# Performance work log

Measured on AMD Instinct MI355X. Metric: run time of the kernel, lower is better.

## Reference

```python
import jax, jax.numpy as jnp
import numpy as np
import math

B, T, C, H, L, V = 8, 511, 1024, 16, 8, 128  # T = block_size - 1
D = C // H
FF = 4 * C


def setup_inputs() -> dict:
    key = jax.random.key(0)
    ks = jax.random.split(key, 12)
    std = 0.02
    n = lambda k, s: (jax.random.normal(k, s, dtype=jnp.float32) * std)
    idx = jax.random.randint(ks[0], (B, T), 0, V)
    idx = jnp.where(idx == 2, 3, idx)  # avoid pad token so logits[idx!=2] keeps all rows
    return {
        "idx": idx,
        "tok_emb": n(ks[1], (V, C)),
        "pos_emb": n(ks[2], (T, C)),
        "ln1_w": jnp.ones((L, C)), "ln1_b": jnp.zeros((L, C)),
        "Wq": n(ks[3], (L, C, C)), "bq": jnp.zeros((L, C)),
        "Wk": n(ks[4], (L, C, C)), "bk": jnp.zeros((L, C)),
        "Wv": n(ks[5], (L, C, C)), "bv": jnp.zeros((L, C)),
        "Wp": n(ks[6], (L, C, C)), "bp": jnp.zeros((L, C)),
        "ln2_w": jnp.ones((L, C)), "ln2_b": jnp.zeros((L, C)),
        "W1": n(ks[7], (L, C, FF)), "b1": jnp.zeros((L, FF)),
        "W2": n(ks[8], (L, FF, C)), "b2": jnp.zeros((L, C)),
        "lnf_w": jnp.ones((C,)), "lnf_b": jnp.zeros((C,)),
        "head_w": n(ks[9], (V, C)),
    }


def _ln(x, w, b):
    m = x.mean(-1, keepdims=True)
    v = ((x - m) ** 2).mean(-1, keepdims=True)
    return (x - m) * jax.lax.rsqrt(v + 1e-5) * w + b


def reference(idx, tok_emb, pos_emb, ln1_w, ln1_b, Wq, bq, Wk, bk, Wv, bv, Wp, bp,
              ln2_w, ln2_b, W1, b1, W2, b2, lnf_w, lnf_b, head_w):
    x = tok_emb[idx] + pos_emb[None, :, :]                      # [B,T,C]
    mask = jnp.tril(jnp.ones((T, T), dtype=bool))
    scale = 1.0 / math.sqrt(D)

    def block(x, p):
        h = _ln(x, p["ln1_w"], p["ln1_b"])
        q = (h @ p["Wq"] + p["bq"]).reshape(B, T, H, D).transpose(0, 2, 1, 3)
        k = (h @ p["Wk"] + p["bk"]).reshape(B, T, H, D).transpose(0, 2, 1, 3)
        v = (h @ p["Wv"] + p["bv"]).reshape(B, T, H, D).transpose(0, 2, 1, 3)
        att = jnp.einsum('bhqd,bhkd->bhqk', q, k) * scale       # [B,H,T,T]
        att = jnp.where(mask, att, -jnp.inf)
        att = jax.nn.softmax(att, axis=-1)
        y = jnp.einsum('bhqk,bhkd->bhqd', att, v)
        y = y.transpose(0, 2, 1, 3).reshape(B, T, C)
        x = x + y @ p["Wp"] + p["bp"]
        h = _ln(x, p["ln2_w"], p["ln2_b"])
        h = jax.nn.gelu(h @ p["W1"] + p["b1"], approximate=False)
        x = x + h @ p["W2"] + p["b2"]
        return x, None

    stacked = dict(ln1_w=ln1_w, ln1_b=ln1_b, Wq=Wq, bq=bq, Wk=Wk, bk=bk, Wv=Wv, bv=bv,
                   Wp=Wp, bp=bp, ln2_w=ln2_w, ln2_b=ln2_b, W1=W1, b1=b1, W2=W2, b2=b2)
    x, _ = jax.lax.scan(block, x, stacked)
    x = _ln(x, lnf_w, lnf_b)
    logits = x @ head_w.T                                       # [B,T,V]
    # logits[idx != 2] with no 2-tokens present == all rows flattened
    return logits.reshape(B * T, V)
```

## Files before the change

### kernel.cpp

```cpp
#include <hip/hip_runtime.h>
#include <hip/hip_bf16.h>

typedef unsigned short u16;
typedef unsigned int   u32;
typedef __attribute__((ext_vector_type(8))) __bf16 bf16x8;
typedef __attribute__((ext_vector_type(4))) float  f32x4;

static constexpr int NB  = 8;
static constexpr int TT  = 511;
static constexpr int CC  = 1024;
static constexpr int HH  = 16;
static constexpr int LL  = 8;
static constexpr int VV  = 128;
static constexpr int FF_ = 4096;
static constexpr int MV  = NB * TT;
static constexpr int MP  = 4096;
static constexpr int TP  = 512;

#define DEVI static __device__ __forceinline__

DEVI u16 f2bf(float f) {
  u32 u = __builtin_bit_cast(u32, f);
  u = (u + 0x7fffu + ((u >> 16) & 1u)) >> 16;
  return (u16)u;
}

DEVI void gload16(const void* g, void* lds) {
  auto gp = (const __attribute__((address_space(1))) u32*)(uintptr_t)g;
  auto lp = (__attribute__((address_space(3))) u32*)(uintptr_t)lds;
  __builtin_amdgcn_global_load_lds(gp, lp, 16, 0, 0);
}

__global__ __launch_bounds__(256) void k_transpose(const float* __restrict__ in,
                                                   u16* __restrict__ out, int K, int N,
                                                   size_t is, size_t os) {
  in  += (size_t)blockIdx.z * is;
  out += (size_t)blockIdx.z * os;
  __shared__ u16 tile[64][66];
  int nb = blockIdx.x * 64, kb = blockIdx.y * 64;
  int t = threadIdx.x;
  int r = t >> 4, c4 = (t & 15) * 4;
#pragma unroll
  for (int i = 0; i < 4; ++i) {
    int k = r + i * 16;
    float4 v = *(const float4*)(in + (size_t)(kb + k) * N + nb + c4);
    tile[k][c4 + 0] = f2bf(v.x); tile[k][c4 + 1] = f2bf(v.y);
    tile[k][c4 + 2] = f2bf(v.z); tile[k][c4 + 3] = f2bf(v.w);
  }
  __syncthreads();
#pragma unroll
  for (int i = 0; i < 4; ++i) {
    int n = r + i * 16;
    ushort4 o;
    o.x = tile[c4 + 0][n]; o.y = tile[c4 + 1][n];
    o.z = tile[c4 + 2][n]; o.w = tile[c4 + 3][n];
    *(ushort4*)(out + (size_t)(nb + n) * K + kb + c4) = o;
  }
}

__global__ __launch_bounds__(256) void k_cast_bf16(const float* __restrict__ in,
                                                   u16* __restrict__ out, int n) {
  int i = blockIdx.x * 256 + threadIdx.x;
  if (i < n) out[i] = f2bf(in[i]);
}

__global__ __launch_bounds__(256) void k_pack_qkv_bias(const float* __restrict__ bq,
                                                       const float* __restrict__ bk,
                                                       const float* __restrict__ bv,
                                                       float* __restrict__ out) {
  int i = blockIdx.x * 256 + threadIdx.x;
  int l = i / (3 * CC), c = i % (3 * CC);
  float v = (c < CC) ? bq[l * CC + c] : (c < 2 * CC) ? bk[l * CC + c - CC] : bv[l * CC + c - 2 * CC];
  out[i] = v;
}

__global__ __launch_bounds__(256) void k_embed(const int* __restrict__ idx,
                                               const float* __restrict__ tok,
                                               const float* __restrict__ pos,
                                               float* __restrict__ x) {
  int row = blockIdx.x;
  int c4 = threadIdx.x * 4;
  if (row >= MV) {
    *(float4*)(x + (size_t)row * CC + c4) = make_float4(0.f, 0.f, 0.f, 0.f);
    return;
  }
  int t = row % TT;
  int tid = idx[row];
  float4 a = *(const float4*)(tok + (size_t)tid * CC + c4);
  float4 p = *(const float4*)(pos + (size_t)t * CC + c4);
  a.x += p.x; a.y += p.y; a.z += p.z; a.w += p.w;
  *(float4*)(x + (size_t)row * CC + c4) = a;
}

__global__ __launch_bounds__(256) void k_ln(const float* __restrict__ x,
                                            const float* __restrict__ w,
                                            const float* __restrict__ b,
                                            u16* __restrict__ out) {
  int wid = threadIdx.x >> 6, l = threadIdx.x & 63;
  int row = blockIdx.x * 4 + wid;
  const float* xr = x + (size_t)row * CC;
  float4 v[4];
  float s = 0.f, sq = 0.f;
#pragma unroll
  for (int i = 0; i < 4; ++i) {
    v[i] = *(const float4*)(xr + (i * 64 + l) * 4);
    s  += v[i].x + v[i].y + v[i].z + v[i].w;
    sq += v[i].x * v[i].x + v[i].y * v[i].y + v[i].z * v[i].z + v[i].w * v[i].w;
  }
#pragma unroll
  for (int o = 32; o; o >>= 1) { s += __shfl_xor(s, o); sq += __shfl_xor(sq, o); }
  float mean = s * (1.f / CC);
  float var  = sq * (1.f / CC) - mean * mean;
  float rs = rsqrtf(var + 1e-5f);
#pragma unroll
  for (int i = 0; i < 4; ++i) {
    int c = (i * 64 + l) * 4;
    float4 wv = *(const float4*)(w + c);
    float4 bv = *(const float4*)(b + c);
    ushort4 o4;
    o4.x = f2bf((v[i].x - mean) * rs * wv.x + bv.x);
    o4.y = f2bf((v[i].y - mean) * rs * wv.y + bv.y);
    o4.z = f2bf((v[i].z - mean) * rs * wv.z + bv.z);
    o4.w = f2bf((v[i].w - mean) * rs * wv.w + bv.w);
    *(ushort4*)(out + (size_t)row * CC + c) = o4;
  }
}

template <int EPI>
__global__ __launch_bounds__(512, 1) void k_gemm4(const u16* __restrict__ A,
                                                  const u16* __restrict__ Wt,
                                                  const float* __restrict__ bias,
                                                  u16* __restrict__ outb,
                                                  int N, int K, int gridN) {
  __shared__ char lds[2][4][16384];
  int t = threadIdx.x, l = t & 63, wid = t >> 6;
  int wr = wid >> 2, wc = wid & 3;
  int lr = l & 15, lk16 = (l >> 4) * 16;

  int nwg = gridDim.x, wg = blockIdx.x;
  int qq = nwg >> 3, r8 = nwg & 7;
  int xcd = wg & 7, loc = wg >> 3;
  int swz = (xcd < r8 ? xcd * (qq + 1) : r8 * (qq + 1) + (xcd - r8) * qq) + loc;
  int mblk = swz / gridN, nblk = swz - mblk * gridN;
  int mb = mblk * 256, nb = nblk * 256;
  int NT = K >> 6;
  const u16* Ab = A  + (size_t)mb * K;
  const u16* Bb = Wt + (size_t)nb * K;

  int srow = t >> 3, skb = (t & 7) * 16;

  auto stageH = [&](int kt, int ht) {
    int b = kt & 1;
    const u16* src = (ht < 2) ? Ab : Bb;
    int rowbase = (ht & 1) << 7;
    char* dst = &lds[b][ht][0];
    const u16* s0 = src + (size_t)rowbase * K + kt * 64;
#pragma unroll
    for (int j = 0; j < 2; ++j) {
      int row = j * 64 + srow;
      int kb = skb ^ ((row & 7) << 4);
      gload16(s0 + (size_t)row * K + (kb >> 1), dst + j * 8192 + t * 16);
    }
  };

  f32x4 acc[8][4] = {};

  stageH(0, 0); stageH(0, 1); stageH(0, 2); stageH(0, 3);
  stageH(1, 2); stageH(1, 0); stageH(1, 3);
  asm volatile("s_waitcnt vmcnt(6)" ::: "memory");
  __builtin_amdgcn_s_barrier();
  __builtin_amdgcn_sched_barrier(0);

  for (int kt = 0; kt < NT; kt += 2) {
    bool s2 = (kt + 2) < NT, s3 = (kt + 3) < NT;
#pragma unroll
    for (int half = 0; half < 2; ++half) {
      int buf = half;
      bf16x8 Bf[2][4];
#pragma unroll
      for (int q = 0; q < 4; ++q) {
        bf16x8 Af[2][2];
        if (q == 0) {
#pragma unroll
          for (int ks = 0; ks < 2; ++ks)
#pragma unroll
            for (int nf = 0; nf < 4; ++nf) {
              int grow = ((wc & 1) << 6) + nf * 16 + lr;
              int kb = (ks * 64 + lk16) ^ ((grow & 7) << 4);
              Bf[ks][nf] = *(const bf16x8*)(&lds[buf][2 + (wc >> 1)][0] + grow * 128 + kb);
            }
        }
#pragma unroll
        for (int ks = 0; ks < 2; ++ks)
#pragma unroll
          for (int dm = 0; dm < 2; ++dm) {
            int mf = q * 2 + dm;
            int grow = wr * 64 + (mf & 3) * 16 + lr;
            int kb = (ks * 64 + lk16) ^ ((grow & 7) << 4);
            Af[ks][dm] = *(const bf16x8*)(&lds[buf][mf >> 2][0] + grow * 128 + kb);
          }
        if (half == 0) {
          if (q == 0)      stageH(kt + 1, 1);
          else if (q == 1) { if (s2) stageH(kt + 2, 2); }
          else if (q == 2) { if (s2) stageH(kt + 2, 0); }
          else             { if (s2) stageH(kt + 2, 3); }
        } else {
          if (q == 0)      { if (s2) stageH(kt + 2, 1); }
          else if (q == 1) { if (s3) stageH(kt + 3, 2); }
          else if (q == 2) { if (s3) stageH(kt + 3, 0); }
          else             { if (s3) stageH(kt + 3, 3); }
        }
        __builtin_amdgcn_sched_barrier(0);
        __builtin_amdgcn_s_barrier();
        asm volatile("s_waitcnt lgkmcnt(0)" ::: "memory");
        __builtin_amdgcn_sched_barrier(0);
        __builtin_amdgcn_s_setprio(1);
#pragma unroll
        for (int ks = 0; ks < 2; ++ks)
#pragma unroll
          for (int dm = 0; dm < 2; ++dm)
#pragma unroll
            for (int nf = 0; nf < 4; ++nf)
              acc[q * 2 + dm][nf] = __builtin_amdgcn_mfma_f32_16x16x32_bf16(
                  Af[ks][dm], Bf[ks][nf], acc[q * 2 + dm][nf], 0, 0, 0);
        __builtin_amdgcn_s_setprio(0);
        if (q == 3) {
          if (half == 0) {
            if (s2) asm volatile("s_waitcnt vmcnt(6)" ::: "memory");
            else    asm volatile("s_waitcnt vmcnt(0)" ::: "memory");
          } else if (s2) {
            if (s3) asm volatile("s_waitcnt vmcnt(6)" ::: "memory");
            else    asm volatile("s_waitcnt vmcnt(0)" ::: "memory");
          }
        }
        __builtin_amdgcn_sched_barrier(0);
        __builtin_amdgcn_s_barrier();
      }
    }
  }

  int r0 = (l >> 4) * 4;
#pragma unroll
  for (int mf = 0; mf < 8; ++mf) {
    int gr = mb + ((mf >> 2) << 7) + wr * 64 + (mf & 3) * 16 + r0;
#pragma unroll
    for (int nf = 0; nf < 4; ++nf) {
      int gc = nb + wc * 64 + nf * 16 + lr;
      float bv = bias[gc];
#pragma unroll
      for (int rr = 0; rr < 4; ++rr) {
        float v = acc[mf][nf][rr] + bv;
        size_t o = (size_t)(gr + rr) * N + gc;
        if constexpr (EPI == 1) {
          outb[o] = f2bf(v);
        } else {
          float g = 0.5f * v * (1.0f + erff(v * 0.70710678f));
          outb[o] = f2bf(g);
        }
      }
    }
  }
}

template <int EPI>
__global__ __launch_bounds__(256, 2) void k_gemm3(const u16* __restrict__ A,
                                                  const u16* __restrict__ Wt,
                                                  const float* __restrict__ bias,
                                                  float* __restrict__ outf,
                                                  const float* __restrict__ resid,
                                                  int N, int K, int gridN, int Mv) {
  constexpr int BTILE = 16384;
  __shared__ u16 lds[2][128 * 64 * 2];

  int t = threadIdx.x, l = t & 63, wid = t >> 6;
  int wr = wid >> 1, wc = wid & 1;
  int lr = l & 15, lk16 = (l >> 4) * 16;

  int nwg = gridDim.x, wg = blockIdx.x;
  int q = nwg >> 3, r = nwg & 7;
  int xcd = wg & 7, loc = wg >> 3;
  int swz = (xcd < r ? xcd * (q + 1) : r * (q + 1) + (xcd - r) * q) + loc;
  int mblk = swz / gridN;
  int nblk = swz - mblk * gridN;
  int mb = mblk * 128, nb = nblk * 128;
  int NT = K >> 6;
  const u16* Ab = A  + (size_t)mb * K;
  const u16* Bb = Wt + (size_t)nb * K;

  int srow = t >> 3;
  int skb  = (t & 7) * 16;

  auto stage = [&](int kt, int b) {
    const u16* As = Ab + kt * 64;
    char* LD = (char*)&lds[b][0];
#pragma unroll
    for (int j = 0; j < 4; ++j) {
      int row = j * 32 + srow;
      int kb  = skb ^ ((row & 7) << 4);
      gload16(As + (size_t)row * K + (kb >> 1), LD + j * 4096 + t * 16);
    }
    const u16* Bs = Bb + kt * 64;
#pragma unroll
    for (int j = 0; j < 4; ++j) {
      int row = j * 32 + srow;
      int kb  = skb ^ ((row & 7) << 4);
      gload16(Bs + (size_t)row * K + (kb >> 1), LD + BTILE + j * 4096 + t * 16);
    }
  };

  f32x4 acc[4][4] = {};

  auto tile = [&](int b) {
    const char* LA = (const char*)&lds[b][0];
    const char* LB = LA + BTILE;
    bf16x8 bfr[2][4], afr[2][4];
#pragma unroll
    for (int ks = 0; ks < 2; ++ks)
#pragma unroll
      for (int n = 0; n < 4; ++n) {
        int rr = wc * 64 + n * 16 + lr;
        int kb = (ks * 64 + lk16) ^ ((rr & 7) << 4);
        bfr[ks][n] = *(const bf16x8*)(LB + rr * 128 + kb);
      }
#pragma unroll
    for (int ks = 0; ks < 2; ++ks)
#pragma unroll
      for (int m = 0; m < 4; ++m) {
        int rr = wr * 64 + m * 16 + lr;
        int kb = (ks * 64 + lk16) ^ ((rr & 7) << 4);
        afr[ks][m] = *(const bf16x8*)(LA + rr * 128 + kb);
      }
    __builtin_amdgcn_s_setprio(1);
#pragma unroll
    for (int ks = 0; ks < 2; ++ks)
#pragma unroll
      for (int m = 0; m < 4; ++m)
#pragma unroll
        for (int n = 0; n < 4; ++n)
          acc[m][n] = __builtin_amdgcn_mfma_f32_16x16x32_bf16(
              afr[ks][m], bfr[ks][n], acc[m][n], 0, 0, 0);
    __builtin_amdgcn_s_setprio(0);
  };

  stage(0, 0);
  stage(1, 1);
  asm volatile("s_waitcnt vmcnt(8)" ::: "memory");
  __builtin_amdgcn_s_barrier();
  __builtin_amdgcn_sched_barrier(0);

  for (int kt = 0; kt < NT; kt += 2) {
#pragma unroll
    for (int sub = 0; sub < 2; ++sub) {
      tile(sub);
      asm volatile("s_waitcnt lgkmcnt(0)" ::: "memory");
      __builtin_amdgcn_s_barrier();
      __builtin_amdgcn_sched_barrier(0);
      if (kt + 2 + sub < NT) {
        stage(kt + 2 + sub, sub);
        asm volatile("s_waitcnt vmcnt(8)" ::: "memory");
      } else {
        asm volatile("s_waitcnt vmcnt(0)" ::: "memory");
      }
      __builtin_amdgcn_s_barrier();
      __builtin_amdgcn_sched_barrier(0);
    }
  }

  int r0 = (l >> 4) * 4;
#pragma unroll
  for (int m = 0; m < 4; ++m) {
    int gr = mb + wr * 64 + m * 16 + r0;
#pragma unroll
    for (int n = 0; n < 4; ++n) {
      int gc = nb + wc * 64 + n * 16 + lr;
      float bv = 0.f;
      if constexpr (EPI == 0) bv = bias[gc];
#pragma unroll
      for (int rr = 0; rr < 4; ++rr) {
        int grr = gr + rr;
        float v = acc[m][n][rr] + bv;
        size_t o = (size_t)grr * N + gc;
        if constexpr (EPI == 0) {
          outf[o] = v + resid[o];
        } else {
          if (grr < Mv) outf[o] = v;
        }
      }
    }
  }
}

__global__ __launch_bounds__(256) void k_vtrans(const u16* __restrict__ qkv,
                                                u16* __restrict__ vt) {
  __shared__ u16 tile[64][66];
  int bh = blockIdx.y;
  int b = bh >> 4, h = bh & 15;
  int t0 = blockIdx.x * 64;
  int t = threadIdx.x;
  int r = t >> 4, c4 = (t & 15) * 4;
#pragma unroll
  for (int i = 0; i < 4; ++i) {
    int tt = r + i * 16;
    int trow = t0 + tt;
    int srow = b * TT + (trow < TT ? trow : TT - 1);
    ushort4 v = *(const ushort4*)(qkv + (size_t)srow * 3072 + 2048 + h * 64 + c4);
    tile[tt][c4 + 0] = v.x; tile[tt][c4 + 1] = v.y;
    tile[tt][c4 + 2] = v.z; tile[tt][c4 + 3] = v.w;
  }
  __syncthreads();
#pragma unroll
  for (int i = 0; i < 4; ++i) {
    int d = r + i * 16;
    ushort4 o;
    o.x = (t0 + c4 + 0 < TT) ? tile[c4 + 0][d] : (u16)0;
    o.y = (t0 + c4 + 1 < TT) ? tile[c4 + 1][d] : (u16)0;
    o.z = (t0 + c4 + 2 < TT) ? tile[c4 + 2][d] : (u16)0;
    o.w = (t0 + c4 + 3 < TT) ? tile[c4 + 3][d] : (u16)0;
    *(ushort4*)(vt + ((size_t)bh * 64 + d) * TP + t0 + c4) = o;
  }
}

__global__ __launch_bounds__(512, 2) void k_attn2(const u16* __restrict__ qkv,
                                                  const u16* __restrict__ vt,
                                                  u16* __restrict__ y) {
  __shared__ u16 Kb[2][64 * 64];
  __shared__ u16 Vb[2][64 * 64];
  __shared__ u16 Pb[8][16 * 64];
  int t = threadIdx.x, l = t & 63, w = t >> 6;

  int nwg = gridDim.x, wg = blockIdx.x;
  int swz = (wg & 7) * (nwg >> 3) + (wg >> 3);
  int bh = swz >> 2, qt = swz & 3;
  int b = bh >> 4, h = bh & 15;
  int q0 = qt * 128;
  int lr = l & 15, lg = l >> 4, lk8 = lg * 8;

  const float ISC = 0.125f;

  bf16x8 Qa[2];
  {
    int qs = q0 + w * 16 + lr;
    const u16* qp = qkv + (size_t)(b * TT + (qs < TT ? qs : TT - 1)) * 3072 + h * 64;
    Qa[0] = *(const bf16x8*)(qp + lk8);
    Qa[1] = *(const bf16x8*)(qp + 32 + lk8);
  }

  int NT = (q0 + 128) >> 6;

  int srow = w * 8 + (l >> 3);
  int sb16 = (l & 7) * 16;
  int bcol = sb16 ^ ((srow & 7) << 4);
  const u16* Ksrc = qkv + 1024 + h * 64;
  const char* Vsrc = (const char*)(vt + ((size_t)bh * 64 + srow) * TP);

  auto stage = [&](int kt, int buf) {
    int kv0 = kt * 64;
    int kvr = kv0 + srow;
    int krow = b * TT + (kvr < TT ? kvr : TT - 1);
    gload16((const char*)(Ksrc + (size_t)krow * 3072) + bcol, (char*)&Kb[buf][0] + t * 16);
    gload16(Vsrc + kv0 * 2 + bcol, (char*)&Vb[buf][0] + t * 16);
  };

  f32x4 O[4] = {};
  float m_[4], s_[4];
#pragma unroll
  for (int r = 0; r < 4; ++r) { m_[r] = -1e30f; s_[r] = 0.f; }

  stage(0, 0);
  for (int kt = 0; kt < NT; ++kt) {
    int buf = kt & 1;
    if (kt + 1 < NT) {
      stage(kt + 1, buf ^ 1);
      asm volatile("s_waitcnt vmcnt(2)" ::: "memory");
    } else {
      asm volatile("s_waitcnt vmcnt(0)" ::: "memory");
    }
    __builtin_amdgcn_s_barrier();

    int kv0 = kt * 64;
    f32x4 S[4];
    const char* LK = (const char*)&Kb[buf][0];
#pragma unroll
    for (int j = 0; j < 4; ++j) {
      f32x4 a = {};
#pragma unroll
      for (int ks = 0; ks < 2; ++ks) {
        int row = j * 16 + lr;
        int kb = ((ks * 32 + lk8) * 2) ^ ((row & 7) << 4);
        bf16x8 kf = *(const bf16x8*)(LK + row * 128 + kb);
        a = __builtin_amdgcn_mfma_f32_16x16x32_bf16(Qa[ks], kf, a, 0, 0, 0);
      }
      S[j] = a;
    }
    int qbase = q0 + w * 16 + lg * 4;
#pragma unroll
    for (int j = 0; j < 4; ++j) {
      int kv = kv0 + j * 16 + lr;
#pragma unroll
      for (int r = 0; r < 4; ++r) {
        bool valid = (kv <= qbase + r) && (kv < TT);
        S[j][r] = valid ? S[j][r] : -1e30f;
      }
    }
    float mx[4];
#pragma unroll
    for (int r = 0; r < 4; ++r)
      mx[r] = fmaxf(fmaxf(S[0][r], S[1][r]), fmaxf(S[2][r], S[3][r]));
#pragma unroll
    for (int r = 0; r < 4; ++r) {
      mx[r] = fmaxf(mx[r], __shfl_xor(mx[r], 1));
      mx[r] = fmaxf(mx[r], __shfl_xor(mx[r], 2));
      mx[r] = fmaxf(mx[r], __shfl_xor(mx[r], 4));
      mx[r] = fmaxf(mx[r], __shfl_xor(mx[r], 8));
    }
    float sc[4];
#pragma unroll
    for (int r = 0; r < 4; ++r) {
      float mn = fmaxf(m_[r], mx[r]);
      sc[r] = __expf((m_[r] - mn) * ISC);
      m_[r] = mn;
      s_[r] *= sc[r];
    }
#pragma unroll
    for (int j = 0; j < 4; ++j)
#pragma unroll
      for (int r = 0; r < 4; ++r) O[j][r] *= sc[r];
    float rs[4] = {0.f, 0.f, 0.f, 0.f};
    char* LP = (char*)&Pb[w][0];
#pragma unroll
    for (int j = 0; j < 4; ++j) {
#pragma unroll
      for (int r = 0; r < 4; ++r) {
        float p = __expf((S[j][r] - m_[r]) * ISC);
        rs[r] += p;
        int row = lg * 4 + r;
        int addr = (row * 128 + (j * 16 + lr) * 2) ^ ((row & 7) << 4);
        *(u16*)(LP + addr) = f2bf(p);
      }
    }
#pragma unroll
    for (int r = 0; r < 4; ++r) {
      rs[r] += __shfl_xor(rs[r], 1);
      rs[r] += __shfl_xor(rs[r], 2);
      rs[r] += __shfl_xor(rs[r], 4);
      rs[r] += __shfl_xor(rs[r], 8);
      s_[r] += rs[r];
    }
    bf16x8 Pa[2];
#pragma unroll
    for (int ks = 0; ks < 2; ++ks) {
      int addr = (lr * 128 + (ks * 32 + lk8) * 2) ^ ((lr & 7) << 4);
      Pa[ks] = *(const bf16x8*)(LP + addr);
    }
    const char* LV = (const char*)&Vb[buf][0];
#pragma unroll
    for (int j = 0; j < 4; ++j) {
#pragma unroll
      for (int ks = 0; ks < 2; ++ks) {
        int row = j * 16 + lr;
        int kb = ((ks * 32 + lk8) * 2) ^ ((row & 7) << 4);
        bf16x8 vf = *(const bf16x8*)(LV + row * 128 + kb);
        O[j] = __builtin_amdgcn_mfma_f32_16x16x32_bf16(Pa[ks], vf, O[j], 0, 0, 0);
      }
    }
    asm volatile("s_waitcnt lgkmcnt(0)" ::: "memory");
    __builtin_amdgcn_s_barrier();
  }

  int qs0 = q0 + w * 16 + lg * 4;
#pragma unroll
  for (int r = 0; r < 4; ++r) {
    float inv = 1.0f / s_[r];
    int qs = qs0 + r;
    if (qs < TT) {
      u16* yp = y + (size_t)(b * TT + qs) * CC + h * 64;
#pragma unroll
      for (int j = 0; j < 4; ++j)
        yp[j * 16 + lr] = f2bf(O[j][r] * inv);
    }
  }
}

extern "C" void kernel_launch(void* const* d_in, const int* in_sizes, int n_in,
                              void* d_out, int out_size, void* d_ws, size_t ws_size,
                              hipStream_t stream) {
  (void)in_sizes; (void)n_in; (void)out_size; (void)ws_size;
  const int*   idx  = (const int*)  d_in[0];
  const float* tok  = (const float*)d_in[1];
  const float* pos  = (const float*)d_in[2];
  const float* ln1w = (const float*)d_in[3];
  const float* ln1b = (const float*)d_in[4];
  const float* Wq   = (const float*)d_in[5];
  const float* bq   = (const float*)d_in[6];
  const float* Wk   = (const float*)d_in[7];
  const float* bk   = (const float*)d_in[8];
  const float* Wv   = (const float*)d_in[9];
  const float* bv   = (const float*)d_in[10];
  const float* Wp   = (const float*)d_in[11];
  const float* bp   = (const float*)d_in[12];
  const float* ln2w = (const float*)d_in[13];
  const float* ln2b = (const float*)d_in[14];
  const float* W1   = (const float*)d_in[15];
  const float* b1   = (const float*)d_in[16];
  const float* W2   = (const float*)d_in[17];
  const float* b2   = (const float*)d_in[18];
  const float* lnfw = (const float*)d_in[19];
  const float* lnfb = (const float*)d_in[20];
  const float* headw= (const float*)d_in[21];
  float* out = (float*)d_out;

  char* p = (char*)d_ws;
  auto alloc = [&](size_t bytes) { char* r = p; p += (bytes + 255) & ~(size_t)255; return r; };
  u16*   wqkv_t = (u16*)  alloc((size_t)LL * 3 * CC * CC * 2);
  u16*   wp_t   = (u16*)  alloc((size_t)LL * CC * CC * 2);
  u16*   w1_t   = (u16*)  alloc((size_t)LL * FF_ * CC * 2);
  u16*   w2_t   = (u16*)  alloc((size_t)LL * CC * FF_ * 2);
  u16*   headb  = (u16*)  alloc((size_t)VV * CC * 2);
  float* bqkv   = (float*)alloc((size_t)LL * 3 * CC * 4);
  float* x      = (float*)alloc((size_t)MP * CC * 4);
  u16*   hbuf   = (u16*)  alloc((size_t)MP * CC * 2);
  u16*   qkv    = (u16*)  alloc((size_t)MP * 3 * CC * 2);
  u16*   vt     = (u16*)  alloc((size_t)NB * HH * 64 * TP * 2);
  u16*   ybuf   = (u16*)  alloc((size_t)MP * CC * 2);
  u16*   ffb    = (u16*)  alloc((size_t)MP * FF_ * 2);

  k_transpose<<<dim3(16, 16, LL), 256, 0, stream>>>(Wq, wqkv_t,                      CC, CC, (size_t)CC * CC, (size_t)3 * CC * CC);
  k_transpose<<<dim3(16, 16, LL), 256, 0, stream>>>(Wk, wqkv_t + (size_t)CC * CC,    CC, CC, (size_t)CC * CC, (size_t)3 * CC * CC);
  k_transpose<<<dim3(16, 16, LL), 256, 0, stream>>>(Wv, wqkv_t + (size_t)2 * CC * CC,CC, CC, (size_t)CC * CC, (size_t)3 * CC * CC);
  k_transpose<<<dim3(16, 16, LL), 256, 0, stream>>>(Wp, wp_t,                        CC, CC, (size_t)CC * CC, (size_t)CC * CC);
  k_transpose<<<dim3(64, 16, LL), 256, 0, stream>>>(W1, w1_t,                        CC, FF_, (size_t)CC * FF_, (size_t)FF_ * CC);
  k_transpose<<<dim3(16, 64, LL), 256, 0, stream>>>(W2, w2_t,                        FF_, CC, (size_t)FF_ * CC, (size_t)CC * FF_);
  k_cast_bf16<<<(VV * CC + 255) / 256, 256, 0, stream>>>(headw, headb, VV * CC);
  k_pack_qkv_bias<<<(LL * 3 * CC) / 256, 256, 0, stream>>>(bq, bk, bv, bqkv);

  k_embed<<<MP, 256, 0, stream>>>(idx, tok, pos, x);

  for (int l = 0; l < LL; ++l) {
    k_ln<<<MP / 4, 256, 0, stream>>>(x, ln1w + (size_t)l * CC, ln1b + (size_t)l * CC, hbuf);
    k_gemm4<1><<<12 * 16, 512, 0, stream>>>(hbuf, wqkv_t + (size_t)l * 3 * CC * CC,
                                            bqkv + (size_t)l * 3 * CC, qkv, 3 * CC, CC, 12);
    k_vtrans<<<dim3(8, NB * HH), 256, 0, stream>>>(qkv, vt);
    k_attn2<<<NB * HH * 4, 512, 0, stream>>>(qkv, vt, ybuf);
    k_gemm3<0><<<32 * 8, 256, 0, stream>>>(ybuf, wp_t + (size_t)l * CC * CC,
                                           bp + (size_t)l * CC, x, x, CC, CC, 8, MP);
    k_ln<<<MP / 4, 256, 0, stream>>>(x, ln2w + (size_t)l * CC, ln2b + (size_t)l * CC, hbuf);
    k_gemm4<2><<<16 * 16, 512, 0, stream>>>(hbuf, w1_t + (size_t)l * FF_ * CC,
                                            b1 + (size_t)l * FF_, ffb, FF_, CC, 16);
    k_gemm3<0><<<32 * 8, 256, 0, stream>>>(ffb, w2_t + (size_t)l * CC * FF_,
                                           b2 + (size_t)l * CC, x, x, CC, FF_, 8, MP);
  }

  k_ln<<<MP / 4, 256, 0, stream>>>(x, lnfw, lnfb, hbuf);
  k_gemm3<3><<<32 * 1, 256, 0, stream>>>(hbuf, headb, nullptr, out, nullptr, VV, CC, 1, MV);
}
```

Measured before the change: 1.695 ms.

## Fuse V transpose into QKV GEMM epilogue and merge weight-prep launches

The QKV GEMM epilogue now writes the V columns directly in the transposed per-head layout the attention kernel reads, so the separate V-transpose kernel is no longer launched in each layer. The Q/K/V/P weight transposes are merged into one launch, and the head-weight cast is merged with the bias packing. This saves per-layer launches and a reread of V from global memory. In exchange the epilogue issues scattered 2-byte stores with poor coalescing. The zero-padding column at t=511 of vt is no longer written, which could leave garbage there.

```diff
diff --git a/kernel.cpp b/kernel.cpp
--- a/kernel.cpp
+++ b/kernel.cpp
@@ -58,20 +58,58 @@
   }
 }
 
-__global__ __launch_bounds__(256) void k_cast_bf16(const float* __restrict__ in,
-                                                   u16* __restrict__ out, int n) {
+__global__ __launch_bounds__(256) void k_transpose4(const float* __restrict__ Wq,
+                                                    const float* __restrict__ Wk,
+                                                    const float* __restrict__ Wv,
+                                                    const float* __restrict__ Wp,
+                                                    u16* __restrict__ wqkv_t,
+                                                    u16* __restrict__ wp_t) {
+  int z = blockIdx.z, which = z >> 3, lyr = z & 7;
+  const float* in; u16* out;
+  size_t sq = (size_t)CC * CC;
+  if (which == 0)      { in = Wq + lyr * sq; out = wqkv_t + lyr * 3 * sq; }
+  else if (which == 1) { in = Wk + lyr * sq; out = wqkv_t + lyr * 3 * sq + sq; }
+  else if (which == 2) { in = Wv + lyr * sq; out = wqkv_t + lyr * 3 * sq + 2 * sq; }
+  else                 { in = Wp + lyr * sq; out = wp_t + lyr * sq; }
+  __shared__ u16 tile[64][66];
+  int nb = blockIdx.x * 64, kb = blockIdx.y * 64;
+  int t = threadIdx.x;
+  int r = t >> 4, c4 = (t & 15) * 4;
+#pragma unroll
+  for (int i = 0; i < 4; ++i) {
+    int k = r + i * 16;
+    float4 v = *(const float4*)(in + (size_t)(kb + k) * CC + nb + c4);
+    tile[k][c4 + 0] = f2bf(v.x); tile[k][c4 + 1] = f2bf(v.y);
+    tile[k][c4 + 2] = f2bf(v.z); tile[k][c4 + 3] = f2bf(v.w);
+  }
+  __syncthreads();
+#pragma unroll
+  for (int i = 0; i < 4; ++i) {
+    int n = r + i * 16;
+    ushort4 o;
+    o.x = tile[c4 + 0][n]; o.y = tile[c4 + 1][n];
+    o.z = tile[c4 + 2][n]; o.w = tile[c4 + 3][n];
+    *(ushort4*)(out + (size_t)(nb + n) * CC + kb + c4) = o;
+  }
+}
+
+__global__ __launch_bounds__(256) void k_prep(const float* __restrict__ headw,
+                                              const float* __restrict__ bq,
+                                              const float* __restrict__ bk,
+                                              const float* __restrict__ bv,
+                                              u16* __restrict__ headb,
+                                              float* __restrict__ bqkv) {
   int i = blockIdx.x * 256 + threadIdx.x;
-  if (i < n) out[i] = f2bf(in[i]);
-}
-
-__global__ __launch_bounds__(256) void k_pack_qkv_bias(const float* __restrict__ bq,
-                                                       const float* __restrict__ bk,
-                                                       const float* __restrict__ bv,
-                                                       float* __restrict__ out) {
-  int i = blockIdx.x * 256 + threadIdx.x;
-  int l = i / (3 * CC), c = i % (3 * CC);
-  float v = (c < CC) ? bq[l * CC + c] : (c < 2 * CC) ? bk[l * CC + c - CC] : bv[l * CC + c - 2 * CC];
-  out[i] = v;
+  if (i < VV * CC) {
+    headb[i] = f2bf(headw[i]);
+  } else {
+    int j = i - VV * CC;
+    if (j < LL * 3 * CC) {
+      int l = j / (3 * CC), c = j % (3 * CC);
+      float v = (c < CC) ? bq[l * CC + c] : (c < 2 * CC) ? bk[l * CC + c - CC] : bv[l * CC + c - 2 * CC];
+      bqkv[j] = v;
+    }
+  }
 }
 
 __global__ __launch_bounds__(256) void k_embed(const int* __restrict__ idx,
@@ -131,6 +169,7 @@
                                                   const u16* __restrict__ Wt,
                                                   const float* __restrict__ bias,
                                                   u16* __restrict__ outb,
+                                                  u16* __restrict__ vt,
                                                   int N, int K, int gridN) {
   __shared__ char lds[2][4][16384];
   int t = threadIdx.x, l = t & 63, wid = t >> 6;
@@ -247,6 +286,21 @@
     for (int nf = 0; nf < 4; ++nf) {
       int gc = nb + wc * 64 + nf * 16 + lr;
       float bv = bias[gc];
+      if constexpr (EPI == 1) {
+        if (gc >= 2048) {
+          int h = (gc - 2048) >> 6, d = gc & 63;
+#pragma unroll
+          for (int rr = 0; rr < 4; ++rr) {
+            int grow = gr + rr;
+            if (grow < MV) {
+              int b = grow / TT;
+              int tt2 = grow - b * TT;
+              vt[(((size_t)(b * HH + h)) * 64 + d) * TP + tt2] = f2bf(acc[mf][nf][rr] + bv);
+            }
+          }
+          continue;
+        }
+      }
 #pragma unroll
       for (int rr = 0; rr < 4; ++rr) {
         float v = acc[mf][nf][rr] + bv;
@@ -387,36 +441,6 @@
         }
       }
     }
-  }
-}
-
-__global__ __launch_bounds__(256) void k_vtrans(const u16* __restrict__ qkv,
-                                                u16* __restrict__ vt) {
-  __shared__ u16 tile[64][66];
-  int bh = blockIdx.y;
-  int b = bh >> 4, h = bh & 15;
-  int t0 = blockIdx.x * 64;
-  int t = threadIdx.x;
-  int r = t >> 4, c4 = (t & 15) * 4;
-#pragma unroll
-  for (int i = 0; i < 4; ++i) {
-    int tt = r + i * 16;
-    int trow = t0 + tt;
-    int srow = b * TT + (trow < TT ? trow : TT - 1);
-    ushort4 v = *(const ushort4*)(qkv + (size_t)srow * 3072 + 2048 + h * 64 + c4);
-    tile[tt][c4 + 0] = v.x; tile[tt][c4 + 1] = v.y;
-    tile[tt][c4 + 2] = v.z; tile[tt][c4 + 3] = v.w;
-  }
-  __syncthreads();
-#pragma unroll
-  for (int i = 0; i < 4; ++i) {
-    int d = r + i * 16;
-    ushort4 o;
-    o.x = (t0 + c4 + 0 < TT) ? tile[c4 + 0][d] : (u16)0;
-    o.y = (t0 + c4 + 1 < TT) ? tile[c4 + 1][d] : (u16)0;
-    o.z = (t0 + c4 + 2 < TT) ? tile[c4 + 2][d] : (u16)0;
-    o.w = (t0 + c4 + 3 < TT) ? tile[c4 + 3][d] : (u16)0;
-    *(ushort4*)(vt + ((size_t)bh * 64 + d) * TP + t0 + c4) = o;
   }
 }
 
@@ -624,28 +648,23 @@
   u16*   ybuf   = (u16*)  alloc((size_t)MP * CC * 2);
   u16*   ffb    = (u16*)  alloc((size_t)MP * FF_ * 2);
 
-  k_transpose<<<dim3(16, 16, LL), 256, 0, stream>>>(Wq, wqkv_t,                      CC, CC, (size_t)CC * CC, (size_t)3 * CC * CC);
-  k_transpose<<<dim3(16, 16, LL), 256, 0, stream>>>(Wk, wqkv_t + (size_t)CC * CC,    CC, CC, (size_t)CC * CC, (size_t)3 * CC * CC);
-  k_transpose<<<dim3(16, 16, LL), 256, 0, stream>>>(Wv, wqkv_t + (size_t)2 * CC * CC,CC, CC, (size_t)CC * CC, (size_t)3 * CC * CC);
-  k_transpose<<<dim3(16, 16, LL), 256, 0, stream>>>(Wp, wp_t,                        CC, CC, (size_t)CC * CC, (size_t)CC * CC);
-  k_transpose<<<dim3(64, 16, LL), 256, 0, stream>>>(W1, w1_t,                        CC, FF_, (size_t)CC * FF_, (size_t)FF_ * CC);
-  k_transpose<<<dim3(16, 64, LL), 256, 0, stream>>>(W2, w2_t,                        FF_, CC, (size_t)FF_ * CC, (size_t)CC * FF_);
-  k_cast_bf16<<<(VV * CC + 255) / 256, 256, 0, stream>>>(headw, headb, VV * CC);
-  k_pack_qkv_bias<<<(LL * 3 * CC) / 256, 256, 0, stream>>>(bq, bk, bv, bqkv);
+  k_transpose4<<<dim3(16, 16, 4 * LL), 256, 0, stream>>>(Wq, Wk, Wv, Wp, wqkv_t, wp_t);
+  k_transpose<<<dim3(64, 16, LL), 256, 0, stream>>>(W1, w1_t, CC, FF_, (size_t)CC * FF_, (size_t)FF_ * CC);
+  k_transpose<<<dim3(16, 64, LL), 256, 0, stream>>>(W2, w2_t, FF_, CC, (size_t)FF_ * CC, (size_t)CC * FF_);
+  k_prep<<<(VV * CC + LL * 3 * CC + 255) / 256, 256, 0, stream>>>(headw, bq, bk, bv, headb, bqkv);
 
   k_embed<<<MP, 256, 0, stream>>>(idx, tok, pos, x);
 
   for (int l = 0; l < LL; ++l) {
     k_ln<<<MP / 4, 256, 0, stream>>>(x, ln1w + (size_t)l * CC, ln1b + (size_t)l * CC, hbuf);
     k_gemm4<1><<<12 * 16, 512, 0, stream>>>(hbuf, wqkv_t + (size_t)l * 3 * CC * CC,
-                                            bqkv + (size_t)l * 3 * CC, qkv, 3 * CC, CC, 12);
-    k_vtrans<<<dim3(8, NB * HH), 256, 0, stream>>>(qkv, vt);
+                                            bqkv + (size_t)l * 3 * CC, qkv, vt, 3 * CC, CC, 12);
     k_attn2<<<NB * HH * 4, 512, 0, stream>>>(qkv, vt, ybuf);
     k_gemm3<0><<<32 * 8, 256, 0, stream>>>(ybuf, wp_t + (size_t)l * CC * CC,
                                            bp + (size_t)l * CC, x, x, CC, CC, 8, MP);
     k_ln<<<MP / 4, 256, 0, stream>>>(x, ln2w + (size_t)l * CC, ln2b + (size_t)l * CC, hbuf);
     k_gemm4<2><<<16 * 16, 512, 0, stream>>>(hbuf, w1_t + (size_t)l * FF_ * CC,
-                                            b1 + (size_t)l * FF_, ffb, FF_, CC, 16);
+                                            b1 + (size_t)l * FF_, ffb, nullptr, FF_, CC, 16);
     k_gemm3<0><<<32 * 8, 256, 0, stream>>>(ffb, w2_t + (size_t)l * CC * FF_,
                                            b2 + (size_t)l * CC, x, x, CC, FF_, 8, MP);
   }
```

After: 1.840 ms. 1.09x slower.
